# Kernel optimization log

Hardware: AMD Instinct MI355X
Metric: run time of the kernel (lower is better)

The kernel has to match this reference:

```python
import math
import jax, jax.numpy as jnp
import numpy as np

B, S, D, H, F, L = 32, 512, 512, 8, 2048, 4
DH = D // H
ALPHA = 1.0
LN_EPS = 1e-12


def setup_inputs() -> dict:
    key = jax.random.key(0)
    ks = jax.random.split(key, 24)
    n = jax.random.normal
    inp = {
        "hidden_states": n(ks[0], (B, S, D), dtype=jnp.float32),
        "position_bias": n(ks[1], (1, H, S, S), dtype=jnp.float32) * 0.02,
        "timestamp": jnp.sort(jax.random.randint(ks[2], (B, S), 0, 10_000_000), axis=-1).astype(jnp.int64),
        # per-layer stacked BERT params
        "Wq": n(ks[3], (L, D, D), dtype=jnp.float32) * 0.02,
        "bq": jnp.zeros((L, D), dtype=jnp.float32),
        "Wk": n(ks[4], (L, D, D), dtype=jnp.float32) * 0.02,
        "bk": jnp.zeros((L, D), dtype=jnp.float32),
        "Wv": n(ks[5], (L, D, D), dtype=jnp.float32) * 0.02,
        "bv": jnp.zeros((L, D), dtype=jnp.float32),
        "Wo": n(ks[6], (L, D, D), dtype=jnp.float32) * 0.02,
        "bo": jnp.zeros((L, D), dtype=jnp.float32),
        "ln1_g": jnp.ones((L, D), dtype=jnp.float32),
        "ln1_b": jnp.zeros((L, D), dtype=jnp.float32),
        "Wi": n(ks[7], (L, D, F), dtype=jnp.float32) * 0.02,
        "bi": jnp.zeros((L, F), dtype=jnp.float32),
        "Wf": n(ks[8], (L, F, D), dtype=jnp.float32) * 0.02,
        "bf": jnp.zeros((L, D), dtype=jnp.float32),
        "ln2_g": jnp.ones((L, D), dtype=jnp.float32),
        "ln2_b": jnp.zeros((L, D), dtype=jnp.float32),
    }
    return inp


def _layernorm(x, g, b):
    mu = jnp.mean(x, axis=-1, keepdims=True)
    var = jnp.mean(jnp.square(x - mu), axis=-1, keepdims=True)
    return (x - mu) * jax.lax.rsqrt(var + LN_EPS) * g + b


def _encoder(hidden_states, position_bias, timestamp,
             Wq, bq, Wk, bk, Wv, bv, Wo, bo, ln1_g, ln1_b,
             Wi, bi, Wf, bf, ln2_g, ln2_b):
    b_, s_, d_ = hidden_states.shape
    # lag-time scale (encoder path: raw timestamps, minutes)
    t = timestamp.astype(jnp.float32)
    lag = (t[:, :, None] - t[:, None, :]) / (60.0 * 1000.0)  # [B,S,S]
    scale = (math.sqrt(DH) - ALPHA / (jnp.maximum(lag, 0.0) + 1.0) + ALPHA)[:, None, :, :]  # [B,1,S,S]

    x = hidden_states
    for l in range(L):
        q = (x @ Wq[l] + bq[l]).reshape(b_, s_, H, DH)
        k = (x @ Wk[l] + bk[l]).reshape(b_, s_, H, DH)
        v = (x @ Wv[l] + bv[l]).reshape(b_, s_, H, DH)
        scores = jnp.einsum('bqhd,bkhd->bhqk', q, k) / scale + position_bias
        probs = jax.nn.softmax(scores, axis=-1)
        ctx = jnp.einsum('bhqk,bkhd->bqhd', probs, v).reshape(b_, s_, d_)
        attn = _layernorm(ctx @ Wo[l] + bo[l] + x, ln1_g[l], ln1_b[l])
        h = jax.nn.gelu(attn @ Wi[l] + bi[l], approximate=False)
        x = _layernorm(h @ Wf[l] + bf[l] + attn, ln2_g[l], ln2_b[l])
    return x


def reference(hidden_states, position_bias, timestamp,
              Wq, bq, Wk, bk, Wv, bv, Wo, bo, ln1_g, ln1_b,
              Wi, bi, Wf, bf, ln2_g, ln2_b):
    return _encoder(hidden_states, position_bias, timestamp,
                    Wq, bq, Wk, bk, Wv, bv, Wo, bo, ln1_g, ln1_b,
                    Wi, bi, Wf, bf, ln2_g, ln2_b)
```

## Files before the change

### kernel.cpp

```cpp
#include <hip/hip_runtime.h>
#include <stdint.h>

#define B_ 32
#define S_ 512
#define D_ 512
#define H_ 8
#define F_ 2048
#define L_ 4
#define DH_ 64
#define M_ (B_*S_)

typedef unsigned short u16;
typedef float f32x4 __attribute__((ext_vector_type(4)));
typedef short bf16x8 __attribute__((ext_vector_type(8)));

__device__ __forceinline__ u16 f2b(float f) {
  unsigned u = __float_as_uint(f);
  u += 0x7FFFu + ((u >> 16) & 1u);
  return (u16)(u >> 16);
}
__device__ __forceinline__ float b2f(u16 u) {
  return __uint_as_float((unsigned)u << 16);
}
__device__ __forceinline__ void gld16(const void* g, void* l) {
  __builtin_amdgcn_global_load_lds((__attribute__((address_space(1))) void*)(void*)g,
                                   (__attribute__((address_space(3))) void*)l, 16, 0, 0);
}
__device__ __forceinline__ f32x4 mfma16(bf16x8 a, bf16x8 b, f32x4 c) {
  return __builtin_amdgcn_mfma_f32_16x16x32_bf16(a, b, c, 0, 0, 0);
}
__device__ __forceinline__ float gelu_fast(float x) {
  float z = 0.7978845608028654f * fmaf(0.044715f * x, x * x, x);
  float e = __expf(2.0f * z);
  float t = 1.0f - 2.0f * __builtin_amdgcn_rcpf(e + 1.0f);
  return 0.5f * x * (1.0f + t);
}

#define LOG2E 1.4426950408889634f

__global__ __launch_bounds__(256) void transpose_w(const float* __restrict__ in,
                                                   u16* __restrict__ out, int R, int C) {
  __shared__ float tile[32][33];
  const int l = blockIdx.z;
  in  += (size_t)l * R * C;
  out += (size_t)l * R * C;
  const int c0 = blockIdx.x * 32, r0 = blockIdx.y * 32;
  const int tx = threadIdx.x, ty = threadIdx.y;
#pragma unroll
  for (int k = 0; k < 4; k++)
    tile[ty + 8*k][tx] = in[(size_t)(r0 + ty + 8*k) * C + c0 + tx];
  __syncthreads();
#pragma unroll
  for (int k = 0; k < 4; k++)
    out[(size_t)(c0 + ty + 8*k) * R + r0 + tx] = f2b(tile[tx][ty + 8*k]);
}

__global__ __launch_bounds__(256) void prep_x(const float* __restrict__ h,
                                              u16* __restrict__ xb) {
  int i = blockIdx.x * 256 + threadIdx.x;
  float4 v = ((const float4*)h)[i];
  ushort4 u; u.x = f2b(v.x); u.y = f2b(v.y); u.z = f2b(v.z); u.w = f2b(v.w);
  ((ushort4*)xb)[i] = u;
}

__global__ __launch_bounds__(256) void prep_pb(const float* __restrict__ pb,
                                               u16* __restrict__ out) {
  const int n0 = (blockIdx.x * 256 + threadIdx.x) * 4;
  const int rowbase = (n0 >> 9) << 9;
  const int nb = n0 & 511;
  const int blk = (nb >> 6) << 6;
  const int lr_ = (nb >> 2) & 15;
  const float* src = pb + rowbase + blk + lr_;
  ushort4 o;
  o.x = f2b(src[0]  * LOG2E);
  o.y = f2b(src[16] * LOG2E);
  o.z = f2b(src[32] * LOG2E);
  o.w = f2b(src[48] * LOG2E);
  ((ushort4*)out)[n0 >> 2] = o;
}

__global__ __launch_bounds__(256) void prep_inv(const int* __restrict__ ts,
                                                u16* __restrict__ invb) {
  const int b  = blockIdx.x >> 7;
  const int rg = blockIdx.x & 127;
  const int wid = threadIdx.x >> 6, lane = threadIdx.x & 63;
  const int i = rg * 4 + wid;
  const float ti = (float)ts[b*S_ + i];
  const int nblk = (lane >> 3) * 64;
  const int l8   = (lane & 7) * 8;
  u16 o[8];
#pragma unroll
  for (int e = 0; e < 8; e++) {
    const int no = l8 + e;
    const int j  = nblk + (no & 3) * 16 + ((no >> 2) & 15);
    float lag = fmaxf((ti - (float)ts[b*S_ + j]) * (1.0f/60000.0f), 0.0f);
    float iv  = (lag + 1.0f) * __builtin_amdgcn_rcpf(fmaf(lag, 9.0f, 8.0f)) * LOG2E;
    o[e] = (u16)(int)rintf((iv - 0.16f) * 524288.0f);
  }
  ushort4 w0 = {o[0], o[1], o[2], o[3]}, w1 = {o[4], o[5], o[6], o[7]};
  u16* out = invb + (((size_t)(b*S_ + i)) << 9) + lane*8;
  *(ushort4*)out       = w0;
  *(ushort4*)(out + 4) = w1;
}

__device__ __forceinline__ void gemm_core(
    const u16* __restrict__ A, const u16* __restrict__ BT,
    const int N, const int K,
    const float* __restrict__ bias, u16* __restrict__ outb, const int epi)
{
  __shared__ u16 As0[128*64], Bs0[128*64];
  __shared__ u16 As1[128*64], Bs1[128*64];
  const int tid = threadIdx.x;
  const int wid = tid >> 6, lane = tid & 63;
  const int wm = (wid >> 1) * 64, wn = (wid & 1) * 64;
  const int lr = lane & 15, quad = lane >> 4;
  const int m0 = blockIdx.x * 128, n0 = blockIdx.y * 128;
  const int l7 = lane & 7, l3 = lane >> 3;
  const int cc = (l7 ^ l3) * 8;
  const int f8 = lr & 7;

  f32x4 acc[4][4];
#pragma unroll
  for (int i = 0; i < 4; i++)
#pragma unroll
    for (int j = 0; j < 4; j++) acc[i][j] = (f32x4){0.f, 0.f, 0.f, 0.f};

  const u16* Ag = A  + (size_t)(m0 + wid*16 + l3)*K + cc;
  const u16* Bg = BT + (size_t)(n0 + l3*4 + wid)*K + cc;
  const int wo = wid * 1024;

  auto STAGE = [&](int k0, u16* AsB, u16* BsB) {
    u16* AsW = AsB + wo;
    u16* BsW = BsB + wo;
    gld16(Ag + k0,                 AsW);
    gld16(Ag + (size_t)8*K + k0,   AsW + 512);
    gld16(Ag + (size_t)64*K + k0,  AsW + 4096);
    gld16(Ag + (size_t)72*K + k0,  AsW + 4608);
    gld16(Bg + k0,                 BsW);
    gld16(Bg + (size_t)32*K + k0,  BsW + 512);
    gld16(Bg + (size_t)64*K + k0,  BsW + 4096);
    gld16(Bg + (size_t)96*K + k0,  BsW + 4608);
  };
  auto COMPUTE = [&](const u16* AsB, const u16* BsB) {
#pragma unroll
    for (int kh = 0; kh < 2; kh++) {
      bf16x8 af[4], bfr[4];
#pragma unroll
      for (int i = 0; i < 4; i++)
        af[i]  = *(const bf16x8*)(AsB + (wm + i*16 + lr)*64 + (((kh*4 + quad) ^ f8) * 8));
#pragma unroll
      for (int j = 0; j < 4; j++)
        bfr[j] = *(const bf16x8*)(BsB + (wn + j*16 + lr)*64 + (((kh*4 + quad) ^ f8) * 8));
#pragma unroll
      for (int i = 0; i < 4; i++)
#pragma unroll
        for (int j = 0; j < 4; j++)
          acc[i][j] = mfma16(af[i], bfr[j], acc[i][j]);
    }
  };

  const int NT = K >> 6;
  STAGE(0, As0, Bs0);
  __syncthreads();
  for (int t = 0; t < NT; t += 2) {
    STAGE((t + 1) << 6, As1, Bs1);
    COMPUTE(As0, Bs0);
    __syncthreads();
    if (t + 2 < NT) STAGE((t + 2) << 6, As0, Bs0);
    COMPUTE(As1, Bs1);
    __syncthreads();
  }

  const int nb = n0 + wn + lr*4;
  float4 b4 = *(const float4*)(bias + nb);
  float bn[4] = {b4.x, b4.y, b4.z, b4.w};

  if (epi == 3) {
#pragma unroll
    for (int i = 0; i < 4; i++) {
      const int m = m0 + wm + i*16 + quad*4;
      const int bb_ = m >> 9, sr = m & 511;
#pragma unroll
      for (int j = 0; j < 4; j++) {
        const int n = nb + j;
        const int hh = n >> 6, dd = n & 63;
        ushort4 o;
        o.x = f2b(acc[i][j][0] + bn[j]);
        o.y = f2b(acc[i][j][1] + bn[j]);
        o.z = f2b(acc[i][j][2] + bn[j]);
        o.w = f2b(acc[i][j][3] + bn[j]);
        *(ushort4*)(outb + (((size_t)((bb_*H_ + hh)*DH_ + dd)) << 9) + sr) = o;
      }
    }
  } else if (epi == 2) {
#pragma unroll
    for (int i = 0; i < 4; i++) {
#pragma unroll
      for (int r = 0; r < 4; r++) {
        const size_t m = (size_t)(m0 + wm + i*16 + quad*4 + r);
        ushort4 o;
        o.x = f2b(gelu_fast(acc[i][0][r] + bn[0]));
        o.y = f2b(gelu_fast(acc[i][1][r] + bn[1]));
        o.z = f2b(gelu_fast(acc[i][2][r] + bn[2]));
        o.w = f2b(gelu_fast(acc[i][3][r] + bn[3]));
        *(ushort4*)(outb + m*N + nb) = o;
      }
    }
  } else {
#pragma unroll
    for (int i = 0; i < 4; i++) {
#pragma unroll
      for (int r = 0; r < 4; r++) {
        const size_t m = (size_t)(m0 + wm + i*16 + quad*4 + r);
        ushort4 o;
        o.x = f2b(acc[i][0][r] + bn[0]);
        o.y = f2b(acc[i][1][r] + bn[1]);
        o.z = f2b(acc[i][2][r] + bn[2]);
        o.w = f2b(acc[i][3][r] + bn[3]);
        *(ushort4*)(outb + m*N + nb) = o;
      }
    }
  }
}

__global__ __launch_bounds__(256) void gemm_kernel(
    const u16* A, const u16* BT, int N, int K,
    const float* bias, u16* outb, int epi)
{
  gemm_core(A, BT, N, K, bias, outb, epi);
}

__global__ __launch_bounds__(256) void gemm_qkv_kernel(
    const u16* A, const u16* BTq, size_t zstride, int K,
    const float* b0, const float* b1, const float* b2,
    u16* out0, u16* out1, u16* out2)
{
  const int z = blockIdx.z;
  const u16* BT = BTq + (size_t)z * zstride;
  const float* bias = (z == 0) ? b0 : (z == 1) ? b1 : b2;
  u16* outb = (z == 0) ? out0 : (z == 1) ? out1 : out2;
  gemm_core(A, BT, 512, K, bias, outb, (z == 2) ? 3 : 0);
}

__global__ __launch_bounds__(512, 2) void gemm_ln_kernel(
    const u16* __restrict__ A, const u16* __restrict__ BT, const int K,
    const float* __restrict__ bias, const u16* __restrict__ resb,
    const float* __restrict__ g, const float* __restrict__ bta,
    float* __restrict__ outf, u16* __restrict__ outb)
{
  __shared__ u16 As0[64*64],  As1[64*64];
  __shared__ u16 Bs0[512*64], Bs1[512*64];
  float (*red)[8] = (float(*)[8])(void*)As0;
  const int tid = threadIdx.x;
  const int wid = tid >> 6, lane = tid & 63;
  const int wr = wid >> 2, wc = wid & 3;
  const int wm = wr * 32;
  const int lr = lane & 15, quad = lane >> 4;
  const int m0 = blockIdx.x * 64;
  const int l7 = lane & 7, l3 = lane >> 3;
  const int cc = (l7 ^ l3) * 8;
  const int f8 = lr & 7;

  f32x4 acc[2][8];
#pragma unroll
  for (int i = 0; i < 2; i++)
#pragma unroll
    for (int j = 0; j < 8; j++) acc[i][j] = (f32x4){0.f, 0.f, 0.f, 0.f};

  const u16* Ag = A  + (size_t)(m0 + wid*8 + l3)*K + cc;
  const u16* Bg = BT + (size_t)(wid*64 + l3*4)*K + cc;

  auto STAGE = [&](int k0, u16* AsB, u16* BsB) {
    gld16(Ag + k0, AsB + wid*512);
    u16* bw = BsB + wid*4096;
#pragma unroll
    for (int ld = 0; ld < 8; ld++)
      gld16(Bg + (size_t)(32*(ld & 1) + (ld >> 1))*K + k0, bw + ld*512);
  };
  auto COMPUTE = [&](const u16* AsB, const u16* BsB) {
#pragma unroll
    for (int kh = 0; kh < 2; kh++) {
      bf16x8 af[2], bfr[8];
#pragma unroll
      for (int i = 0; i < 2; i++)
        af[i]  = *(const bf16x8*)(AsB + (wm + i*16 + lr)*64 + (((kh*4 + quad) ^ f8) * 8));
#pragma unroll
      for (int j = 0; j < 8; j++)
        bfr[j] = *(const bf16x8*)(BsB + (wc*128 + j*16 + lr)*64 + (((kh*4 + quad) ^ f8) * 8));
#pragma unroll
      for (int i = 0; i < 2; i++)
#pragma unroll
        for (int j = 0; j < 8; j++)
          acc[i][j] = mfma16(af[i], bfr[j], acc[i][j]);
    }
  };

  const int NT = K >> 6;
  STAGE(0, As0, Bs0);
  __syncthreads();
  for (int t = 0; t < NT; t += 2) {
    STAGE((t + 1) << 6, As1, Bs1);
    COMPUTE(As0, Bs0);
    __syncthreads();
    if (t + 2 < NT) STAGE((t + 2) << 6, As0, Bs0);
    COMPUTE(As1, Bs1);
    __syncthreads();
  }

  const int c0 = wc*128 + lr*4;
  float4 bA = *(const float4*)(bias + c0);
  float4 bB = *(const float4*)(bias + c0 + 64);
  float sum[2][4], ssq[2][4];
#pragma unroll
  for (int i = 0; i < 2; i++) {
#pragma unroll
    for (int r = 0; r < 4; r++) {
      const size_t rowg = (size_t)(m0 + wm + i*16 + quad*4 + r);
      ushort4 q0 = *(const ushort4*)(resb + rowg*D_ + c0);
      ushort4 q1 = *(const ushort4*)(resb + rowg*D_ + c0 + 64);
      acc[i][0][r] += bA.x + b2f(q0.x);
      acc[i][1][r] += bA.y + b2f(q0.y);
      acc[i][2][r] += bA.z + b2f(q0.z);
      acc[i][3][r] += bA.w + b2f(q0.w);
      acc[i][4][r] += bB.x + b2f(q1.x);
      acc[i][5][r] += bB.y + b2f(q1.y);
      acc[i][6][r] += bB.z + b2f(q1.z);
      acc[i][7][r] += bB.w + b2f(q1.w);
      float s = 0.f, q = 0.f;
#pragma unroll
      for (int j = 0; j < 8; j++) { float y = acc[i][j][r]; s += y; q += y*y; }
#pragma unroll
      for (int m = 1; m < 16; m <<= 1) { s += __shfl_xor(s, m); q += __shfl_xor(q, m); }
      sum[i][r] = s; ssq[i][r] = q;
    }
  }
  if (lr == 0) {
#pragma unroll
    for (int i = 0; i < 2; i++)
#pragma unroll
      for (int r = 0; r < 4; r++) {
        const int rl = wm + i*16 + quad*4 + r;
        red[rl][wc*2]     = sum[i][r];
        red[rl][wc*2 + 1] = ssq[i][r];
      }
  }
  __syncthreads();

  float4 gA = *(const float4*)(g + c0);
  float4 gB = *(const float4*)(g + c0 + 64);
  float4 aA = *(const float4*)(bta + c0);
  float4 aB = *(const float4*)(bta + c0 + 64);
  float gg[8] = {gA.x, gA.y, gA.z, gA.w, gB.x, gB.y, gB.z, gB.w};
  float bb[8] = {aA.x, aA.y, aA.z, aA.w, aB.x, aB.y, aB.z, aB.w};
#pragma unroll
  for (int i = 0; i < 2; i++) {
#pragma unroll
    for (int r = 0; r < 4; r++) {
      const int rl = wm + i*16 + quad*4 + r;
      const size_t rowg = (size_t)(m0 + rl);
      float4 p0 = *(const float4*)&red[rl][0];
      float4 p1 = *(const float4*)&red[rl][4];
      const float mu = (p0.x + p0.z + p1.x + p1.z) * (1.0f/512.0f);
      const float eq = (p0.y + p0.w + p1.y + p1.w) * (1.0f/512.0f);
      const float rs = rsqrtf(fmaxf(eq - mu*mu, 0.0f) + 1e-12f);
      float o[8];
#pragma unroll
      for (int j = 0; j < 8; j++) o[j] = (acc[i][j][r] - mu) * rs * gg[j] + bb[j];
      ushort4 w0 = {f2b(o[0]), f2b(o[1]), f2b(o[2]), f2b(o[3])};
      ushort4 w1 = {f2b(o[4]), f2b(o[5]), f2b(o[6]), f2b(o[7])};
      *(ushort4*)(outb + rowg*D_ + c0)      = w0;
      *(ushort4*)(outb + rowg*D_ + c0 + 64) = w1;
      if (outf) {
        float4 f0 = {o[0], o[1], o[2], o[3]}, f1 = {o[4], o[5], o[6], o[7]};
        *(float4*)(outf + rowg*D_ + c0)      = f0;
        *(float4*)(outf + rowg*D_ + c0 + 64) = f1;
      }
    }
  }
}

__global__ __launch_bounds__(256, 4) void attn_kernel(
    const u16* __restrict__ qb, const u16* __restrict__ kb, const u16* __restrict__ vt,
    const u16* __restrict__ pb16, const u16* __restrict__ invb, u16* __restrict__ cb)
{
  __shared__ u16 QPs[64*64];
  __shared__ u16 Ks[64*64], Vs[64*64], PBs[64*64], INVs[64*64];
  const int b = blockIdx.x, it = blockIdx.y, h = blockIdx.z;
  const int i0 = it * 64;
  const int tid = threadIdx.x, wid = tid >> 6, lane = tid & 63;
  const int lr = lane & 15, quad = lane >> 4;
  const int l7 = lane & 7, l3 = lane >> 3;
  const int cc = (l7 ^ l3) * 8;
  const int f8 = lr & 7;
  const int rr = wid*8 + l3;

  const u16* qg  = qb + ((size_t)(b*S_ + i0))*D_ + h*DH_;
  const u16* kg  = kb + ((size_t)b*S_)*D_ + h*DH_;
  const u16* vg  = vt + ((size_t)(b*H_ + h)*DH_)*S_;
  const u16* pbg = pb16 + ((size_t)(h*S_ + i0))*S_;
  const u16* ivg = invb + ((size_t)(b*S_ + i0))*S_;

  gld16(qg + (size_t)rr*D_ + cc,        QPs + wid*512);
  gld16(qg + (size_t)(rr+32)*D_ + cc,   QPs + 2048 + wid*512);
  __syncthreads();

  bf16x8 aq0 = *(const bf16x8*)(QPs + (wid*16 + lr)*64 + ((quad ^ f8) * 8));
  bf16x8 aq1 = *(const bf16x8*)(QPs + (wid*16 + lr)*64 + (((quad ^ f8) ^ 4) * 8));
  u16* Pw = QPs + wid*1024;

  f32x4 O[4]; float lacc[4];
#pragma unroll
  for (int dt = 0; dt < 4; dt++) O[dt] = (f32x4){0.f, 0.f, 0.f, 0.f};
#pragma unroll
  for (int r = 0; r < 4; r++) lacc[r] = 0.f;
  const int lrh = lr >> 3;

  for (int t8 = 0; t8 < 8; t8++) {
    const int j0 = t8 * 64;
    gld16(kg + (size_t)(j0+rr)*D_ + cc,       Ks   + wid*512);
    gld16(kg + (size_t)(j0+rr+32)*D_ + cc,    Ks   + 2048 + wid*512);
    gld16(vg + (size_t)rr*S_ + j0 + cc,       Vs   + wid*512);
    gld16(vg + (size_t)(rr+32)*S_ + j0 + cc,  Vs   + 2048 + wid*512);
    gld16(pbg + (size_t)rr*S_ + j0 + cc,      PBs  + wid*512);
    gld16(pbg + (size_t)(rr+32)*S_ + j0 + cc, PBs  + 2048 + wid*512);
    gld16(ivg + (size_t)rr*S_ + j0 + cc,      INVs + wid*512);
    gld16(ivg + (size_t)(rr+32)*S_ + j0 + cc, INVs + 2048 + wid*512);
    __syncthreads();

    f32x4 s[4];
#pragma unroll
    for (int jt = 0; jt < 4; jt++) {
      const u16* kr = Ks + (jt*16 + lr)*64;
      bf16x8 bk0 = *(const bf16x8*)(kr + ((quad ^ f8) * 8));
      bf16x8 bk1 = *(const bf16x8*)(kr + (((quad ^ f8) ^ 4) * 8));
      f32x4 z = (f32x4){0.f, 0.f, 0.f, 0.f};
      z = mfma16(aq0, bk0, z);
      z = mfma16(aq1, bk1, z);
      s[jt] = z;
    }
#pragma unroll
    for (int r = 0; r < 4; r++) {
      const int rowl = quad*4 + r;
      const int r7 = rowl & 7;
      const int tbase = (wid*16 + rowl)*64 + ((((lr >> 1) ^ r7) << 3) | ((lr & 1) << 2));
      ushort4 ivq = *(const ushort4*)(INVs + tbase);
      ushort4 pbq = *(const ushort4*)(PBs + tbase);
      const u16 ive[4] = {ivq.x, ivq.y, ivq.z, ivq.w};
      const u16 pbe[4] = {pbq.x, pbq.y, pbq.z, pbq.w};
      const int pbase = rowl*64;
      float pa = 0.f;
#pragma unroll
      for (int jt = 0; jt < 4; jt++) {
        float iv  = fmaf((float)ive[jt], 0x1p-19f, 0.16f);
        float pbf = b2f(pbe[jt]);
        float p = __builtin_amdgcn_exp2f(fmaf(s[jt][r], iv, pbf));
        pa += p;
        const int idx = (((jt*2 + lrh) ^ r7) * 8) + l7;
        Pw[pbase + idx] = f2b(p);
      }
      lacc[r] += pa;
    }
    bf16x8 ap0 = *(const bf16x8*)(Pw + lr*64 + ((quad ^ f8) * 8));
    bf16x8 ap1 = *(const bf16x8*)(Pw + lr*64 + (((quad ^ f8) ^ 4) * 8));
#pragma unroll
    for (int dt = 0; dt < 4; dt++) {
      const u16* vr = Vs + (dt*16 + lr)*64;
      bf16x8 bv0 = *(const bf16x8*)(vr + ((quad ^ f8) * 8));
      bf16x8 bv1 = *(const bf16x8*)(vr + (((quad ^ f8) ^ 4) * 8));
      O[dt] = mfma16(ap0, bv0, O[dt]);
      O[dt] = mfma16(ap1, bv1, O[dt]);
    }
    __syncthreads();
  }

#pragma unroll
  for (int r = 0; r < 4; r++) {
    float sum = lacc[r];
#pragma unroll
    for (int m = 1; m < 16; m <<= 1) sum += __shfl_xor(sum, m);
    const float inv = __builtin_amdgcn_rcpf(sum);
    const size_t row = (size_t)(b*S_ + i0 + wid*16 + quad*4 + r);
#pragma unroll
    for (int dt = 0; dt < 4; dt++)
      cb[row*D_ + h*DH_ + dt*16 + lr] = f2b(O[dt][r] * inv);
  }
}

extern "C" void kernel_launch(void* const* d_in, const int* in_sizes, int n_in,
                              void* d_out, int out_size, void* d_ws, size_t ws_size,
                              hipStream_t stream)
{
  const float* hidden = (const float*)d_in[0];
  const float* pbias  = (const float*)d_in[1];
  const int*   ts     = (const int*)d_in[2];
  const float* Wq = (const float*)d_in[3];   const float* bq  = (const float*)d_in[4];
  const float* Wk = (const float*)d_in[5];   const float* bk  = (const float*)d_in[6];
  const float* Wv = (const float*)d_in[7];   const float* bv  = (const float*)d_in[8];
  const float* Wo = (const float*)d_in[9];   const float* bo  = (const float*)d_in[10];
  const float* l1g = (const float*)d_in[11]; const float* l1b = (const float*)d_in[12];
  const float* Wi = (const float*)d_in[13];  const float* bi  = (const float*)d_in[14];
  const float* Wf = (const float*)d_in[15];  const float* bfw = (const float*)d_in[16];
  const float* l2g = (const float*)d_in[17]; const float* l2b = (const float*)d_in[18];

  char* w = (char*)d_ws;
  u16* xb    = (u16*)w; w += (size_t)M_*D_*2;
  u16* qb    = (u16*)w; w += (size_t)M_*D_*2;
  u16* kbuf  = (u16*)w; w += (size_t)M_*D_*2;
  u16* vtw   = (u16*)w; w += (size_t)M_*D_*2;
  u16* cbuf  = (u16*)w; w += (size_t)M_*D_*2;
  u16* attnb = (u16*)w; w += (size_t)M_*D_*2;
  u16* WqkvT = (u16*)w; w += (size_t)3*L_*D_*D_*2;
  u16* WoT   = (u16*)w; w += (size_t)L_*D_*D_*2;
  u16* WiT   = (u16*)w; w += (size_t)L_*D_*F_*2;
  u16* WfT   = (u16*)w; w += (size_t)L_*F_*D_*2;
  u16* pbb   = (u16*)w; w += (size_t)H_*S_*S_*2;
  u16* invb  = (u16*)w; w += (size_t)B_*S_*S_*2;
  u16* hb    = qb;

  float* x = (float*)d_out;

  const size_t WD = (size_t)D_*D_;
  const size_t WF = (size_t)D_*F_;
  dim3 tb(32, 8);

  transpose_w<<<dim3(16,16,L_), tb, 0, stream>>>(Wq, WqkvT,           D_, D_);
  transpose_w<<<dim3(16,16,L_), tb, 0, stream>>>(Wk, WqkvT + L_*WD,   D_, D_);
  transpose_w<<<dim3(16,16,L_), tb, 0, stream>>>(Wv, WqkvT + 2*L_*WD, D_, D_);
  transpose_w<<<dim3(16,16,L_), tb, 0, stream>>>(Wo, WoT,             D_, D_);
  transpose_w<<<dim3(64,16,L_), tb, 0, stream>>>(Wi, WiT,             D_, F_);
  transpose_w<<<dim3(16,64,L_), tb, 0, stream>>>(Wf, WfT,             F_, D_);
  prep_x<<<dim3(8192), dim3(256), 0, stream>>>(hidden, xb);
  prep_pb<<<dim3(H_*S_*S_/1024), dim3(256), 0, stream>>>(pbias, pbb);
  prep_inv<<<dim3(B_*S_/4), dim3(256), 0, stream>>>(ts, invb);

  for (int l = 0; l < L_; l++) {
    gemm_qkv_kernel<<<dim3(128,4,3), dim3(256), 0, stream>>>(
        xb, WqkvT + l*WD, (size_t)L_*WD, D_,
        bq + l*D_, bk + l*D_, bv + l*D_, qb, kbuf, vtw);
    attn_kernel<<<dim3(B_,8,H_), dim3(256), 0, stream>>>(qb, kbuf, vtw, pbb, invb, cbuf);
    gemm_ln_kernel<<<dim3(256), dim3(512), 0, stream>>>(
        cbuf, WoT + l*WD, D_, bo + l*D_, xb,
        l1g + l*D_, l1b + l*D_, (float*)nullptr, attnb);
    gemm_kernel<<<dim3(128,16), dim3(256), 0, stream>>>(
        attnb, WiT + l*WF, F_, D_, bi + l*F_, hb, 2);
    gemm_ln_kernel<<<dim3(256), dim3(512), 0, stream>>>(
        hb, WfT + l*WF, F_, bfw + l*D_, attnb,
        l2g + l*D_, l2b + l*D_, (l == 3) ? x : (float*)nullptr, xb);
  }
}
```

Baseline: 978.9 us.

## Prefetch two stages ahead with fine-grained vmcnt waits in GEMM loops

Reworks the double-buffered GEMM main loops so both LDS buffers are filled up front. Each compute step then waits only for its own buffer's loads via s_waitcnt vmcnt plus a raw barrier, instead of a full __syncthreads that drains every load. N and K also become template parameters so loop bounds are compile-time constants. This lets more global-to-LDS traffic overlap with MFMA work, but correctness now depends on hand-counted vmcnt values that must match the exact number of loads issued per STAGE.

```diff
diff --git a/kernel.cpp b/kernel.cpp
--- a/kernel.cpp
+++ b/kernel.cpp
@@ -37,6 +37,10 @@
 }
 
 #define LOG2E 1.4426950408889634f
+#define VMWAIT(n)  asm volatile("s_waitcnt vmcnt(" #n ")" ::: "memory")
+#define LGKM0()    asm volatile("s_waitcnt lgkmcnt(0)" ::: "memory")
+#define SBAR()     __builtin_amdgcn_s_barrier()
+#define SCHED0()   __builtin_amdgcn_sched_barrier(0)
 
 __global__ __launch_bounds__(256) void transpose_w(const float* __restrict__ in,
                                                    u16* __restrict__ out, int R, int C) {
@@ -103,9 +107,9 @@
   *(ushort4*)(out + 4) = w1;
 }
 
+template<int N, int K>
 __device__ __forceinline__ void gemm_core(
     const u16* __restrict__ A, const u16* __restrict__ BT,
-    const int N, const int K,
     const float* __restrict__ bias, u16* __restrict__ outb, const int epi)
 {
   __shared__ u16 As0[128*64], Bs0[128*64];
@@ -159,17 +163,23 @@
     }
   };
 
-  const int NT = K >> 6;
+  constexpr int NT = K >> 6;
   STAGE(0, As0, Bs0);
-  __syncthreads();
-  for (int t = 0; t < NT; t += 2) {
-    STAGE((t + 1) << 6, As1, Bs1);
+  STAGE(64, As1, Bs1);
+  for (int t = 0; t + 2 < NT; t += 2) {
+    VMWAIT(8); SBAR(); SCHED0();
     COMPUTE(As0, Bs0);
-    __syncthreads();
-    if (t + 2 < NT) STAGE((t + 2) << 6, As0, Bs0);
+    LGKM0(); SBAR();
+    STAGE((t + 2) << 6, As0, Bs0);
+    VMWAIT(8); SBAR(); SCHED0();
     COMPUTE(As1, Bs1);
-    __syncthreads();
-  }
+    LGKM0(); SBAR();
+    STAGE((t + 3) << 6, As1, Bs1);
+  }
+  VMWAIT(8); SBAR(); SCHED0();
+  COMPUTE(As0, Bs0);
+  VMWAIT(0); LGKM0(); SBAR(); SCHED0();
+  COMPUTE(As1, Bs1);
 
   const int nb = n0 + wn + lr*4;
   float4 b4 = *(const float4*)(bias + nb);
@@ -223,15 +233,15 @@
   }
 }
 
-__global__ __launch_bounds__(256) void gemm_kernel(
-    const u16* A, const u16* BT, int N, int K,
-    const float* bias, u16* outb, int epi)
+template<int N, int K>
+__global__ __launch_bounds__(256) void gemm_tmpl_kernel(
+    const u16* A, const u16* BT, const float* bias, u16* outb, int epi)
 {
-  gemm_core(A, BT, N, K, bias, outb, epi);
+  gemm_core<N, K>(A, BT, bias, outb, epi);
 }
 
 __global__ __launch_bounds__(256) void gemm_qkv_kernel(
-    const u16* A, const u16* BTq, size_t zstride, int K,
+    const u16* A, const u16* BTq, size_t zstride,
     const float* b0, const float* b1, const float* b2,
     u16* out0, u16* out1, u16* out2)
 {
@@ -239,11 +249,12 @@
   const u16* BT = BTq + (size_t)z * zstride;
   const float* bias = (z == 0) ? b0 : (z == 1) ? b1 : b2;
   u16* outb = (z == 0) ? out0 : (z == 1) ? out1 : out2;
-  gemm_core(A, BT, 512, K, bias, outb, (z == 2) ? 3 : 0);
-}
-
+  gemm_core<512, 512>(A, BT, bias, outb, (z == 2) ? 3 : 0);
+}
+
+template<int K>
 __global__ __launch_bounds__(512, 2) void gemm_ln_kernel(
-    const u16* __restrict__ A, const u16* __restrict__ BT, const int K,
+    const u16* __restrict__ A, const u16* __restrict__ BT,
     const float* __restrict__ bias, const u16* __restrict__ resb,
     const float* __restrict__ g, const float* __restrict__ bta,
     float* __restrict__ outf, u16* __restrict__ outb)
@@ -295,17 +306,24 @@
     }
   };
 
-  const int NT = K >> 6;
+  constexpr int NT = K >> 6;
   STAGE(0, As0, Bs0);
+  STAGE(64, As1, Bs1);
+  for (int t = 0; t + 2 < NT; t += 2) {
+    VMWAIT(9); SBAR(); SCHED0();
+    COMPUTE(As0, Bs0);
+    LGKM0(); SBAR();
+    STAGE((t + 2) << 6, As0, Bs0);
+    VMWAIT(9); SBAR(); SCHED0();
+    COMPUTE(As1, Bs1);
+    LGKM0(); SBAR();
+    STAGE((t + 3) << 6, As1, Bs1);
+  }
+  VMWAIT(9); SBAR(); SCHED0();
+  COMPUTE(As0, Bs0);
+  VMWAIT(0); LGKM0(); SBAR(); SCHED0();
+  COMPUTE(As1, Bs1);
   __syncthreads();
-  for (int t = 0; t < NT; t += 2) {
-    STAGE((t + 1) << 6, As1, Bs1);
-    COMPUTE(As0, Bs0);
-    __syncthreads();
-    if (t + 2 < NT) STAGE((t + 2) << 6, As0, Bs0);
-    COMPUTE(As1, Bs1);
-    __syncthreads();
-  }
 
   const int c0 = wc*128 + lr*4;
   float4 bA = *(const float4*)(bias + c0);
@@ -535,16 +553,16 @@
 
   for (int l = 0; l < L_; l++) {
     gemm_qkv_kernel<<<dim3(128,4,3), dim3(256), 0, stream>>>(
-        xb, WqkvT + l*WD, (size_t)L_*WD, D_,
+        xb, WqkvT + l*WD, (size_t)L_*WD,
         bq + l*D_, bk + l*D_, bv + l*D_, qb, kbuf, vtw);
     attn_kernel<<<dim3(B_,8,H_), dim3(256), 0, stream>>>(qb, kbuf, vtw, pbb, invb, cbuf);
-    gemm_ln_kernel<<<dim3(256), dim3(512), 0, stream>>>(
-        cbuf, WoT + l*WD, D_, bo + l*D_, xb,
+    gemm_ln_kernel<512><<<dim3(256), dim3(512), 0, stream>>>(
+        cbuf, WoT + l*WD, bo + l*D_, xb,
         l1g + l*D_, l1b + l*D_, (float*)nullptr, attnb);
-    gemm_kernel<<<dim3(128,16), dim3(256), 0, stream>>>(
-        attnb, WiT + l*WF, F_, D_, bi + l*F_, hb, 2);
-    gemm_ln_kernel<<<dim3(256), dim3(512), 0, stream>>>(
-        hb, WfT + l*WF, F_, bfw + l*D_, attnb,
+    gemm_tmpl_kernel<2048,512><<<dim3(128,16), dim3(256), 0, stream>>>(
+        attnb, WiT + l*WF, bi + l*F_, hb, 2);
+    gemm_ln_kernel<2048><<<dim3(256), dim3(512), 0, stream>>>(
+        hb, WfT + l*WF, bfw + l*D_, attnb,
         l2g + l*D_, l2b + l*D_, (l == 3) ? x : (float*)nullptr, xb);
   }
 }
```

Result: faster. 932.8 us (-4.7%).
